# Optimization experiments

Measured on AMD Instinct MI355X. Metric: run time of the kernel, lower is better.

The kernel has to match this reference:

```python
import jax, jax.numpy as jnp
import numpy as np

B, N, D, H = 4, 1024, 1024, 16
NP = N - 1  # prototypes; +1 CLS slot -> n_valid == N
HD = D // H
LN_EPS = 1e-5


def _build_spatial_sim(key):
    centers = jax.random.uniform(key, (NP, 2), dtype=jnp.float32) * 10.0
    diff = centers[:, None, :] - centers[None, :, :]
    d2 = jnp.sum(diff * diff, axis=-1)           # squared pairwise distance
    dist = jnp.sqrt(d2)
    sigma = dist.mean()                           # spatial_sigma = mean cdist
    sim = jnp.exp(-d2 / (2.0 * sigma * sigma))
    sim = sim / sim.max()
    ext = jnp.zeros((NP + 1, NP + 1), dtype=jnp.float32)
    ext = ext.at[0, :].set(1.0).at[:, 0].set(1.0).at[1:, 1:].set(sim)
    return ext


def setup_inputs() -> dict:
    key = jax.random.key(0)
    kc, kx, kq, kp = jax.random.split(key, 4)
    spatial_sim = _build_spatial_sim(kc)          # [N, N] buffer
    x = jax.random.normal(kx, (B, N, D), dtype=jnp.float32)
    gamma = jnp.ones((D,), dtype=jnp.float32)
    beta = jnp.zeros((D,), dtype=jnp.float32)
    w_qkv = jax.random.normal(kq, (D, 3 * D), dtype=jnp.float32) * 0.02
    w_proj = jax.random.normal(kp, (D, D), dtype=jnp.float32) * 0.02
    b_proj = jnp.zeros((D,), dtype=jnp.float32)
    swl = jnp.float32(np.log(0.3 / 0.7))          # inverse_sigmoid(0.3)
    return {"x": x, "gamma": gamma, "beta": beta, "w_qkv": w_qkv,
            "w_proj": w_proj, "b_proj": b_proj,
            "spatial_weight_logit": swl, "spatial_sim": spatial_sim}


def reference(x, gamma, beta, w_qkv, w_proj, b_proj, spatial_weight_logit, spatial_sim):
    b, n, d = x.shape
    scale = HD ** (-0.5)
    # LayerNorm (biased variance, eps=1e-5)
    mu = x.mean(axis=-1, keepdims=True)
    var = jnp.mean((x - mu) ** 2, axis=-1, keepdims=True)
    x_norm = (x - mu) / jnp.sqrt(var + LN_EPS) * gamma + beta
    # QKV projection -> [B, H, N, HD] each
    qkv = (x_norm @ w_qkv).reshape(b, n, 3, H, HD)
    qkv = jnp.transpose(qkv, (2, 0, 3, 1, 4))
    q, k, v = qkv[0], qkv[1], qkv[2]
    scores = jnp.einsum('bhnd,bhmd->bhnm', q, k) * scale
    alpha = jax.nn.sigmoid(spatial_weight_logit)
    # blend feature attention with fixed spatial similarity, then softmax
    attn = jax.nn.softmax((1.0 - alpha) * scores + alpha * spatial_sim[None, None], axis=-1)
    out = jnp.einsum('bhnm,bhmd->bhnd', attn, v)
    out = jnp.transpose(out, (0, 2, 1, 3)).reshape(b, n, d)
    out = out @ w_proj + b_proj
    return x + out
```

## Files before the change

kernel.cpp:

```cpp
#include <hip/hip_runtime.h>

#define Bz 4
#define Nn 1024
#define Dd 1024
#define Hh 16
#define HD 64
#define SCALE 0.125f
#define LN_EPS 1e-5f

typedef __attribute__((ext_vector_type(8))) __bf16 bf16x8;
typedef __attribute__((ext_vector_type(4))) float f32x4;

static __device__ inline unsigned short f2bf(float f) {
    unsigned int u = __float_as_uint(f);
    u += 0x7fffu + ((u >> 16) & 1u);
    return (unsigned short)(u >> 16);
}

static __device__ inline float bf2f(unsigned short s) {
    return __uint_as_float((unsigned)s << 16);
}

static __device__ inline bf16x8 ldfrag(const unsigned short* p) {
    return *(const bf16x8*)p;
}

static __device__ __forceinline__ void glds16(const unsigned short* g, unsigned short* l) {
    __builtin_amdgcn_global_load_lds((const __attribute__((address_space(1))) void*)g,
                                     (__attribute__((address_space(3))) void*)l, 16, 0, 0);
}

__global__ __launch_bounds__(256) void ln_kernel(const float* __restrict__ x,
                                                 const float* __restrict__ gamma,
                                                 const float* __restrict__ beta,
                                                 unsigned short* __restrict__ xn) {
    int row = blockIdx.x;
    int t = threadIdx.x;
    const float* xr = x + (size_t)row * Dd;
    float4 v = ((const float4*)xr)[t];
    float s = v.x + v.y + v.z + v.w;
    float ss = v.x * v.x + v.y * v.y + v.z * v.z + v.w * v.w;
    for (int o = 32; o > 0; o >>= 1) {
        s += __shfl_down(s, o);
        ss += __shfl_down(ss, o);
    }
    __shared__ float red[8];
    int wid = t >> 6;
    if ((t & 63) == 0) { red[wid * 2] = s; red[wid * 2 + 1] = ss; }
    __syncthreads();
    float tot = red[0] + red[2] + red[4] + red[6];
    float tot2 = red[1] + red[3] + red[5] + red[7];
    float mu = tot * (1.0f / Dd);
    float var = tot2 * (1.0f / Dd) - mu * mu;
    float inv = rsqrtf(var + LN_EPS);
    float4 g = ((const float4*)gamma)[t];
    float4 b = ((const float4*)beta)[t];
    ushort4 o4;
    o4.x = f2bf((v.x - mu) * inv * g.x + b.x);
    o4.y = f2bf((v.y - mu) * inv * g.y + b.y);
    o4.z = f2bf((v.z - mu) * inv * g.z + b.z);
    o4.w = f2bf((v.w - mu) * inv * g.w + b.w);
    ((ushort4*)(xn + (size_t)row * Dd))[t] = o4;
}

__global__ __launch_bounds__(256) void transpose_bf16(const float* __restrict__ in,
                                                      unsigned short* __restrict__ out,
                                                      int rows, int cols) {
    __shared__ float tile[32][33];
    int c0 = blockIdx.x * 32, r0 = blockIdx.y * 32;
    int tx = threadIdx.x, ty = threadIdx.y;
    for (int i = 0; i < 32; i += 8)
        tile[ty + i][tx] = in[(size_t)(r0 + ty + i) * cols + c0 + tx];
    __syncthreads();
    for (int i = 0; i < 32; i += 8)
        out[(size_t)(c0 + ty + i) * rows + r0 + tx] = f2bf(tile[tx][ty + i]);
}

__global__ __launch_bounds__(256) void conv_bf16(const float* __restrict__ in,
                                                 unsigned short* __restrict__ out) {
    int i = blockIdx.x * 256 + threadIdx.x;
    float4 v = ((const float4*)in)[i];
    ushort4 o;
    o.x = f2bf(v.x); o.y = f2bf(v.y); o.z = f2bf(v.z); o.w = f2bf(v.w);
    ((ushort4*)out)[i] = o;
}

__global__ __launch_bounds__(256) void gemm_qkv(const unsigned short* __restrict__ A,
                                                const unsigned short* __restrict__ Bt,
                                                unsigned short* __restrict__ qb,
                                                unsigned short* __restrict__ kb,
                                                unsigned short* __restrict__ vtb) {
    __shared__ unsigned short sA[4096], sB[4096];
    int tid = threadIdx.x;
    int w = tid >> 6, lane = tid & 63, lrow = lane & 15, quad = lane >> 4;
    int wm = w >> 1, wn = w & 1;
    int rowbase = blockIdx.y * 128;
    int colbase = blockIdx.x * 128;

    int srow = tid >> 2;
    int kcl = tid & 3;
    int kcg = (kcl - (srow >> 1)) & 3;
    const unsigned short* gA0 = A + (size_t)(rowbase + srow) * 1024 + kcg * 8;
    const unsigned short* gA1 = gA0 + (size_t)64 * 1024;
    const unsigned short* gB0 = Bt + (size_t)(colbase + srow) * 1024 + kcg * 8;
    const unsigned short* gB1 = gB0 + (size_t)64 * 1024;
    unsigned short* lA = sA + w * 512;
    unsigned short* lB = sB + w * 512;

    int ssw = (quad + (lrow >> 1)) & 3;
    const unsigned short* fa = sA + (wm * 64 + lrow) * 32 + ssw * 8;
    const unsigned short* fb = sB + (wn * 64 + lrow) * 32 + ssw * 8;

    f32x4 acc[4][4];
    #pragma unroll
    for (int i = 0; i < 4; i++)
        #pragma unroll
        for (int j = 0; j < 4; j++)
            acc[i][j] = (f32x4){0.f, 0.f, 0.f, 0.f};

    for (int k0 = 0; k0 < 1024; k0 += 32) {
        __syncthreads();
        glds16(gA0 + k0, lA);
        glds16(gA1 + k0, lA + 2048);
        glds16(gB0 + k0, lB);
        glds16(gB1 + k0, lB + 2048);
        __syncthreads();
        bf16x8 a[4], b[4];
        #pragma unroll
        for (int i = 0; i < 4; i++) a[i] = *(const bf16x8*)(fa + i * 512);
        #pragma unroll
        for (int j = 0; j < 4; j++) b[j] = *(const bf16x8*)(fb + j * 512);
        #pragma unroll
        for (int i = 0; i < 4; i++)
            #pragma unroll
            for (int j = 0; j < 4; j++)
                acc[i][j] = __builtin_amdgcn_mfma_f32_16x16x32_bf16(a[i], b[j], acc[i][j], 0, 0, 0);
    }

    #pragma unroll
    for (int j = 0; j < 4; j++) {
        int col = colbase + wn * 64 + j * 16 + lrow;
        int s = col >> 10, rem = col & 1023;
        int h = rem >> 6, e = rem & 63;
        #pragma unroll
        for (int i = 0; i < 4; i++) {
            #pragma unroll
            for (int r = 0; r < 4; r++) {
                int R = rowbase + wm * 64 + i * 16 + quad * 4 + r;
                int bb = R >> 10, n = R & 1023;
                unsigned short val = f2bf(acc[i][j][r]);
                if (s == 0)
                    qb[(((size_t)(bb * Hh + h)) * Nn + n) * HD + e] = val;
                else if (s == 1)
                    kb[(((size_t)(bb * Hh + h)) * Nn + n) * HD + e] = val;
                else
                    vtb[(((size_t)(bb * Hh + h)) * HD + e) * Nn + n] = val;
            }
        }
    }
}

__global__ __launch_bounds__(256) void gemm_proj(const unsigned short* __restrict__ A,
                                                 const unsigned short* __restrict__ Bt,
                                                 const float* __restrict__ bias,
                                                 const float* __restrict__ x,
                                                 float* __restrict__ out) {
    __shared__ unsigned short sA[4096], sB[4096];
    int tid = threadIdx.x;
    int w = tid >> 6, lane = tid & 63, lrow = lane & 15, quad = lane >> 4;
    int wm = w >> 1, wn = w & 1;
    int rowbase = blockIdx.y * 128;
    int colbase = blockIdx.x * 128;

    int srow = tid >> 2;
    int kcl = tid & 3;
    int kcg = (kcl - (srow >> 1)) & 3;
    const unsigned short* gA0 = A + (size_t)(rowbase + srow) * 1024 + kcg * 8;
    const unsigned short* gA1 = gA0 + (size_t)64 * 1024;
    const unsigned short* gB0 = Bt + (size_t)(colbase + srow) * 1024 + kcg * 8;
    const unsigned short* gB1 = gB0 + (size_t)64 * 1024;
    unsigned short* lA = sA + w * 512;
    unsigned short* lB = sB + w * 512;

    int ssw = (quad + (lrow >> 1)) & 3;
    const unsigned short* fa = sA + (wm * 64 + lrow) * 32 + ssw * 8;
    const unsigned short* fb = sB + (wn * 64 + lrow) * 32 + ssw * 8;

    f32x4 acc[4][4];
    #pragma unroll
    for (int i = 0; i < 4; i++)
        #pragma unroll
        for (int j = 0; j < 4; j++)
            acc[i][j] = (f32x4){0.f, 0.f, 0.f, 0.f};

    for (int k0 = 0; k0 < 1024; k0 += 32) {
        __syncthreads();
        glds16(gA0 + k0, lA);
        glds16(gA1 + k0, lA + 2048);
        glds16(gB0 + k0, lB);
        glds16(gB1 + k0, lB + 2048);
        __syncthreads();
        bf16x8 a[4], b[4];
        #pragma unroll
        for (int i = 0; i < 4; i++) a[i] = *(const bf16x8*)(fa + i * 512);
        #pragma unroll
        for (int j = 0; j < 4; j++) b[j] = *(const bf16x8*)(fb + j * 512);
        #pragma unroll
        for (int i = 0; i < 4; i++)
            #pragma unroll
            for (int j = 0; j < 4; j++)
                acc[i][j] = __builtin_amdgcn_mfma_f32_16x16x32_bf16(a[i], b[j], acc[i][j], 0, 0, 0);
    }

    #pragma unroll
    for (int j = 0; j < 4; j++) {
        int col = colbase + wn * 64 + j * 16 + lrow;
        float bc = bias[col];
        #pragma unroll
        for (int i = 0; i < 4; i++) {
            #pragma unroll
            for (int r = 0; r < 4; r++) {
                int R = rowbase + wm * 64 + i * 16 + quad * 4 + r;
                out[(size_t)R * 1024 + col] = acc[i][j][r] + bc + x[(size_t)R * 1024 + col];
            }
        }
    }
}

#define PSTR 72
__global__ __launch_bounds__(256) void attn_kernel(const unsigned short* __restrict__ qb,
                                                   const unsigned short* __restrict__ kb,
                                                   const unsigned short* __restrict__ vtb,
                                                   const unsigned short* __restrict__ simb,
                                                   const float* __restrict__ swl,
                                                   unsigned short* __restrict__ aout) {
    int h = blockIdx.y, bb = blockIdx.z;
    int n0 = blockIdx.x * 128;
    int tid = threadIdx.x;
    int w = tid >> 6, lane = tid & 63;
    int lrow = lane & 15, quad = lane >> 4;
    const unsigned short* q = qb + ((size_t)(bb * Hh + h)) * Nn * HD;
    const unsigned short* k = kb + ((size_t)(bb * Hh + h)) * Nn * HD;
    const unsigned short* vt = vtb + ((size_t)(bb * Hh + h)) * HD * Nn;
    float alpha = 1.f / (1.f + __expf(-swl[0]));
    float c1 = (1.f - alpha) * SCALE;

    __shared__ unsigned short sK[4096];
    __shared__ unsigned short sV[4096];
    __shared__ unsigned short sP[128 * PSTR];

    int qr0 = n0 + w * 32;
    bf16x8 qf[2][2];
    #pragma unroll
    for (int g = 0; g < 2; g++) {
        qf[g][0] = ldfrag(q + (size_t)(qr0 + g * 16 + lrow) * HD + quad * 8);
        qf[g][1] = ldfrag(q + (size_t)(qr0 + g * 16 + lrow) * HD + 32 + quad * 8);
    }

    f32x4 o[2][4];
    #pragma unroll
    for (int g = 0; g < 2; g++)
        #pragma unroll
        for (int et = 0; et < 4; et++) o[g][et] = (f32x4){0.f, 0.f, 0.f, 0.f};
    float rsum[2] = {0.f, 0.f};

    int bs0 = (quad + (lrow >> 1)) & 7;
    int bs1 = (4 + quad + (lrow >> 1)) & 7;
    unsigned short* sPw = sP + (w * 32) * PSTR;

    for (int m0 = 0; m0 < 1024; m0 += 64) {
        __syncthreads();
        #pragma unroll
        for (int i = 0; i < 2; i++) {
            int slot = i * 256 + tid;
            int row = slot >> 3;
            int cg = ((slot & 7) - (row >> 1)) & 7;
            glds16(k + (size_t)(m0 + row) * HD + cg * 8, sK + i * 2048 + w * 512);
        }
        #pragma unroll
        for (int i = 0; i < 2; i++) {
            int slot = i * 256 + tid;
            int row = slot >> 3;
            int cg = ((slot & 7) - (row >> 1)) & 7;
            glds16(vt + (size_t)row * Nn + m0 + cg * 8, sV + i * 2048 + w * 512);
        }
        ushort4 sm[4][2];
        #pragma unroll
        for (int ks = 0; ks < 4; ks++)
            #pragma unroll
            for (int g = 0; g < 2; g++)
                sm[ks][g] = *(const ushort4*)(simb + (size_t)(qr0 + g * 16 + lrow) * Nn
                                              + m0 + ks * 16 + quad * 4);
        __syncthreads();

        #pragma unroll
        for (int ks = 0; ks < 4; ks++) {
            const unsigned short* kr = sK + (ks * 16 + lrow) * 64;
            bf16x8 ak0 = *(const bf16x8*)(kr + bs0 * 8);
            bf16x8 ak1 = *(const bf16x8*)(kr + bs1 * 8);
            #pragma unroll
            for (int g = 0; g < 2; g++) {
                f32x4 c = (f32x4){0.f, 0.f, 0.f, 0.f};
                c = __builtin_amdgcn_mfma_f32_16x16x32_bf16(ak0, qf[g][0], c, 0, 0, 0);
                c = __builtin_amdgcn_mfma_f32_16x16x32_bf16(ak1, qf[g][1], c, 0, 0, 0);
                const unsigned short* smp = (const unsigned short*)&sm[ks][g];
                float e0 = __expf(c1 * c[0] + alpha * bf2f(smp[0]));
                float e1 = __expf(c1 * c[1] + alpha * bf2f(smp[1]));
                float e2 = __expf(c1 * c[2] + alpha * bf2f(smp[2]));
                float e3 = __expf(c1 * c[3] + alpha * bf2f(smp[3]));
                rsum[g] += (e0 + e1) + (e2 + e3);
                uint2 pk;
                pk.x = (__float_as_uint(e0) >> 16) | (__float_as_uint(e1) & 0xffff0000u);
                pk.y = (__float_as_uint(e2) >> 16) | (__float_as_uint(e3) & 0xffff0000u);
                *(uint2*)(sPw + (g * 16 + lrow) * PSTR + ks * 16 + quad * 4) = pk;
            }
        }

        #pragma unroll
        for (int ms = 0; ms < 2; ms++) {
            bf16x8 pa[2];
            #pragma unroll
            for (int g = 0; g < 2; g++)
                pa[g] = *(const bf16x8*)(sPw + (g * 16 + lrow) * PSTR + ms * 32 + quad * 8);
            #pragma unroll
            for (int et = 0; et < 4; et++) {
                int e = et * 16 + lrow;
                int slot = (ms * 4 + quad + (e >> 1)) & 7;
                bf16x8 vb = *(const bf16x8*)(sV + e * 64 + slot * 8);
                #pragma unroll
                for (int g = 0; g < 2; g++)
                    o[g][et] = __builtin_amdgcn_mfma_f32_16x16x32_bf16(pa[g], vb, o[g][et], 0, 0, 0);
            }
        }
    }

    #pragma unroll
    for (int g = 0; g < 2; g++) {
        rsum[g] += __shfl_xor(rsum[g], 16);
        rsum[g] += __shfl_xor(rsum[g], 32);
    }

    #pragma unroll
    for (int g = 0; g < 2; g++)
        #pragma unroll
        for (int r = 0; r < 4; r++) {
            float inv = 1.f / __shfl(rsum[g], quad * 4 + r);
            int qn = qr0 + g * 16 + quad * 4 + r;
            #pragma unroll
            for (int et = 0; et < 4; et++)
                aout[((size_t)bb * Nn + qn) * Dd + h * HD + et * 16 + lrow]
                    = f2bf(o[g][et][r] * inv);
        }
}

extern "C" void kernel_launch(void* const* d_in, const int* in_sizes, int n_in,
                              void* d_out, int out_size, void* d_ws, size_t ws_size,
                              hipStream_t stream) {
    const float* x      = (const float*)d_in[0];
    const float* gamma  = (const float*)d_in[1];
    const float* beta   = (const float*)d_in[2];
    const float* w_qkv  = (const float*)d_in[3];
    const float* w_proj = (const float*)d_in[4];
    const float* b_proj = (const float*)d_in[5];
    const float* swl    = (const float*)d_in[6];
    const float* sim    = (const float*)d_in[7];
    float* out = (float*)d_out;

    unsigned short* ws = (unsigned short*)d_ws;
    unsigned short* xn     = ws;
    unsigned short* wqkvT  = xn + 4194304;
    unsigned short* wprojT = wqkvT + 3145728;
    unsigned short* qb     = wprojT + 1048576;
    unsigned short* kb     = qb + 4194304;
    unsigned short* vtb    = kb + 4194304;
    unsigned short* aout   = vtb + 4194304;
    unsigned short* simb   = xn;

    transpose_bf16<<<dim3(3072 / 32, 1024 / 32), dim3(32, 8), 0, stream>>>(w_qkv, wqkvT, 1024, 3072);
    transpose_bf16<<<dim3(1024 / 32, 1024 / 32), dim3(32, 8), 0, stream>>>(w_proj, wprojT, 1024, 1024);
    ln_kernel<<<4096, 256, 0, stream>>>(x, gamma, beta, xn);
    gemm_qkv<<<dim3(24, 32), 256, 0, stream>>>(xn, wqkvT, qb, kb, vtb);
    conv_bf16<<<1024, 256, 0, stream>>>(sim, simb);
    attn_kernel<<<dim3(8, 16, 4), 256, 0, stream>>>(qb, kb, vtb, simb, swl, aout);
    gemm_proj<<<dim3(8, 32), 256, 0, stream>>>(aout, wprojT, b_proj, x, out);
}
```

Before: 231.5 us.

## Double GEMM K-tile to 64 and stage V-transpose stores through LDS

Both GEMM kernels now load a 64-wide K slice per iteration (twice the shared memory) with an 8-chunk swizzle. This halves the number of barrier pairs and global-to-LDS round trips per output tile. The QKV kernel also splits its epilogue: Q/K blocks write directly, while V blocks transpose through LDS so the transposed V stores become contiguous 8-byte writes instead of scattered 2-byte ones. The larger LDS footprint may lower occupancy.

```diff
diff --git a/kernel.cpp b/kernel.cpp
--- a/kernel.cpp
+++ b/kernel.cpp
@@ -85,31 +85,30 @@
     ((ushort4*)out)[i] = o;
 }
 
+
 __global__ __launch_bounds__(256) void gemm_qkv(const unsigned short* __restrict__ A,
                                                 const unsigned short* __restrict__ Bt,
                                                 unsigned short* __restrict__ qb,
                                                 unsigned short* __restrict__ kb,
                                                 unsigned short* __restrict__ vtb) {
-    __shared__ unsigned short sA[4096], sB[4096];
+    __shared__ unsigned short sA[8192], sB[8192];
     int tid = threadIdx.x;
     int w = tid >> 6, lane = tid & 63, lrow = lane & 15, quad = lane >> 4;
     int wm = w >> 1, wn = w & 1;
     int rowbase = blockIdx.y * 128;
     int colbase = blockIdx.x * 128;
 
-    int srow = tid >> 2;
-    int kcl = tid & 3;
-    int kcg = (kcl - (srow >> 1)) & 3;
-    const unsigned short* gA0 = A + (size_t)(rowbase + srow) * 1024 + kcg * 8;
-    const unsigned short* gA1 = gA0 + (size_t)64 * 1024;
-    const unsigned short* gB0 = Bt + (size_t)(colbase + srow) * 1024 + kcg * 8;
-    const unsigned short* gB1 = gB0 + (size_t)64 * 1024;
+    int srow = tid >> 3;
+    int gch = ((tid & 7) - (srow >> 1)) & 7;
+    const unsigned short* gA = A + (size_t)(rowbase + srow) * 1024 + gch * 8;
+    const unsigned short* gB = Bt + (size_t)(colbase + srow) * 1024 + gch * 8;
     unsigned short* lA = sA + w * 512;
     unsigned short* lB = sB + w * 512;
 
-    int ssw = (quad + (lrow >> 1)) & 3;
-    const unsigned short* fa = sA + (wm * 64 + lrow) * 32 + ssw * 8;
-    const unsigned short* fb = sB + (wn * 64 + lrow) * 32 + ssw * 8;
+    int bs0 = ((quad + (lrow >> 1)) & 7) * 8;
+    int bs1 = ((4 + quad + (lrow >> 1)) & 7) * 8;
+    const unsigned short* fa = sA + (wm * 64 + lrow) * 64;
+    const unsigned short* fb = sB + (wn * 64 + lrow) * 64;
 
     f32x4 acc[4][4];
     #pragma unroll
@@ -118,43 +117,70 @@
         for (int j = 0; j < 4; j++)
             acc[i][j] = (f32x4){0.f, 0.f, 0.f, 0.f};
 
-    for (int k0 = 0; k0 < 1024; k0 += 32) {
-        __syncthreads();
-        glds16(gA0 + k0, lA);
-        glds16(gA1 + k0, lA + 2048);
-        glds16(gB0 + k0, lB);
-        glds16(gB1 + k0, lB + 2048);
-        __syncthreads();
-        bf16x8 a[4], b[4];
-        #pragma unroll
-        for (int i = 0; i < 4; i++) a[i] = *(const bf16x8*)(fa + i * 512);
-        #pragma unroll
-        for (int j = 0; j < 4; j++) b[j] = *(const bf16x8*)(fb + j * 512);
-        #pragma unroll
-        for (int i = 0; i < 4; i++)
-            #pragma unroll
-            for (int j = 0; j < 4; j++)
-                acc[i][j] = __builtin_amdgcn_mfma_f32_16x16x32_bf16(a[i], b[j], acc[i][j], 0, 0, 0);
-    }
-
-    #pragma unroll
-    for (int j = 0; j < 4; j++) {
-        int col = colbase + wn * 64 + j * 16 + lrow;
-        int s = col >> 10, rem = col & 1023;
-        int h = rem >> 6, e = rem & 63;
-        #pragma unroll
-        for (int i = 0; i < 4; i++) {
-            #pragma unroll
-            for (int r = 0; r < 4; r++) {
-                int R = rowbase + wm * 64 + i * 16 + quad * 4 + r;
-                int bb = R >> 10, n = R & 1023;
-                unsigned short val = f2bf(acc[i][j][r]);
-                if (s == 0)
-                    qb[(((size_t)(bb * Hh + h)) * Nn + n) * HD + e] = val;
-                else if (s == 1)
-                    kb[(((size_t)(bb * Hh + h)) * Nn + n) * HD + e] = val;
-                else
-                    vtb[(((size_t)(bb * Hh + h)) * HD + e) * Nn + n] = val;
+    for (int k0 = 0; k0 < 1024; k0 += 64) {
+        __syncthreads();
+        #pragma unroll
+        for (int c = 0; c < 4; c++) {
+            glds16(gA + (size_t)c * 32768 + k0, lA + c * 2048);
+            glds16(gB + (size_t)c * 32768 + k0, lB + c * 2048);
+        }
+        __syncthreads();
+        #pragma unroll
+        for (int s = 0; s < 2; s++) {
+            int bo = s ? bs1 : bs0;
+            bf16x8 a[4], b[4];
+            #pragma unroll
+            for (int i = 0; i < 4; i++) a[i] = *(const bf16x8*)(fa + i * 1024 + bo);
+            #pragma unroll
+            for (int j = 0; j < 4; j++) b[j] = *(const bf16x8*)(fb + j * 1024 + bo);
+            #pragma unroll
+            for (int i = 0; i < 4; i++)
+                #pragma unroll
+                for (int j = 0; j < 4; j++)
+                    acc[i][j] = __builtin_amdgcn_mfma_f32_16x16x32_bf16(a[i], b[j], acc[i][j], 0, 0, 0);
+        }
+    }
+
+    if (colbase < 2048) {
+        #pragma unroll
+        for (int j = 0; j < 4; j++) {
+            int col = colbase + wn * 64 + j * 16 + lrow;
+            int s = col >> 10, rem = col & 1023;
+            int h = rem >> 6, e = rem & 63;
+            unsigned short* dst = (s == 0) ? qb : kb;
+            #pragma unroll
+            for (int i = 0; i < 4; i++) {
+                #pragma unroll
+                for (int r = 0; r < 4; r++) {
+                    int R = rowbase + wm * 64 + i * 16 + quad * 4 + r;
+                    int bb = R >> 10, n = R & 1023;
+                    dst[(((size_t)(bb * Hh + h)) * Nn + n) * HD + e] = f2bf(acc[i][j][r]);
+                }
+            }
+        }
+    } else {
+        int bb = rowbase >> 10;
+        int nbase = (rowbase & 1023) + wm * 64;
+        unsigned short* sc = sA + w * 2048;
+        int er = lane >> 2, nc = lane & 3;
+        #pragma unroll
+        for (int j = 0; j < 4; j++) {
+            __syncthreads();
+            int ebase = colbase + wn * 64 + j * 16 - 2048;
+            int h = ebase >> 6, e0 = ebase & 63;
+            #pragma unroll
+            for (int i = 0; i < 4; i++) {
+                uint2 pk;
+                pk.x = (unsigned)f2bf(acc[i][j][0]) | ((unsigned)f2bf(acc[i][j][1]) << 16);
+                pk.y = (unsigned)f2bf(acc[i][j][2]) | ((unsigned)f2bf(acc[i][j][3]) << 16);
+                *(uint2*)(sc + lrow * 68 + i * 16 + quad * 4) = pk;
+            }
+            __syncthreads();
+            unsigned short* vrow = vtb + ((size_t)((bb * Hh + h) * HD) + e0 + er) * Nn + nbase;
+            #pragma unroll
+            for (int c = 0; c < 4; c++) {
+                uint2 v = *(const uint2*)(sc + er * 68 + c * 16 + nc * 4);
+                *(uint2*)(vrow + c * 16 + nc * 4) = v;
             }
         }
     }
@@ -165,26 +191,24 @@
                                                  const float* __restrict__ bias,
                                                  const float* __restrict__ x,
                                                  float* __restrict__ out) {
-    __shared__ unsigned short sA[4096], sB[4096];
+    __shared__ unsigned short sA[8192], sB[8192];
     int tid = threadIdx.x;
     int w = tid >> 6, lane = tid & 63, lrow = lane & 15, quad = lane >> 4;
     int wm = w >> 1, wn = w & 1;
     int rowbase = blockIdx.y * 128;
     int colbase = blockIdx.x * 128;
 
-    int srow = tid >> 2;
-    int kcl = tid & 3;
-    int kcg = (kcl - (srow >> 1)) & 3;
-    const unsigned short* gA0 = A + (size_t)(rowbase + srow) * 1024 + kcg * 8;
-    const unsigned short* gA1 = gA0 + (size_t)64 * 1024;
-    const unsigned short* gB0 = Bt + (size_t)(colbase + srow) * 1024 + kcg * 8;
-    const unsigned short* gB1 = gB0 + (size_t)64 * 1024;
+    int srow = tid >> 3;
+    int gch = ((tid & 7) - (srow >> 1)) & 7;
+    const unsigned short* gA = A + (size_t)(rowbase + srow) * 1024 + gch * 8;
+    const unsigned short* gB = Bt + (size_t)(colbase + srow) * 1024 + gch * 8;
     unsigned short* lA = sA + w * 512;
     unsigned short* lB = sB + w * 512;
 
-    int ssw = (quad + (lrow >> 1)) & 3;
-    const unsigned short* fa = sA + (wm * 64 + lrow) * 32 + ssw * 8;
-    const unsigned short* fb = sB + (wn * 64 + lrow) * 32 + ssw * 8;
+    int bs0 = ((quad + (lrow >> 1)) & 7) * 8;
+    int bs1 = ((4 + quad + (lrow >> 1)) & 7) * 8;
+    const unsigned short* fa = sA + (wm * 64 + lrow) * 64;
+    const unsigned short* fb = sB + (wn * 64 + lrow) * 64;
 
     f32x4 acc[4][4];
     #pragma unroll
@@ -193,23 +217,28 @@
         for (int j = 0; j < 4; j++)
             acc[i][j] = (f32x4){0.f, 0.f, 0.f, 0.f};
 
-    for (int k0 = 0; k0 < 1024; k0 += 32) {
-        __syncthreads();
-        glds16(gA0 + k0, lA);
-        glds16(gA1 + k0, lA + 2048);
-        glds16(gB0 + k0, lB);
-        glds16(gB1 + k0, lB + 2048);
-        __syncthreads();
-        bf16x8 a[4], b[4];
-        #pragma unroll
-        for (int i = 0; i < 4; i++) a[i] = *(const bf16x8*)(fa + i * 512);
-        #pragma unroll
-        for (int j = 0; j < 4; j++) b[j] = *(const bf16x8*)(fb + j * 512);
-        #pragma unroll
-        for (int i = 0; i < 4; i++)
-            #pragma unroll
-            for (int j = 0; j < 4; j++)
-                acc[i][j] = __builtin_amdgcn_mfma_f32_16x16x32_bf16(a[i], b[j], acc[i][j], 0, 0, 0);
+    for (int k0 = 0; k0 < 1024; k0 += 64) {
+        __syncthreads();
+        #pragma unroll
+        for (int c = 0; c < 4; c++) {
+            glds16(gA + (size_t)c * 32768 + k0, lA + c * 2048);
+            glds16(gB + (size_t)c * 32768 + k0, lB + c * 2048);
+        }
+        __syncthreads();
+        #pragma unroll
+        for (int s = 0; s < 2; s++) {
+            int bo = s ? bs1 : bs0;
+            bf16x8 a[4], b[4];
+            #pragma unroll
+            for (int i = 0; i < 4; i++) a[i] = *(const bf16x8*)(fa + i * 1024 + bo);
+            #pragma unroll
+            for (int j = 0; j < 4; j++) b[j] = *(const bf16x8*)(fb + j * 1024 + bo);
+            #pragma unroll
+            for (int i = 0; i < 4; i++)
+                #pragma unroll
+                for (int j = 0; j < 4; j++)
+                    acc[i][j] = __builtin_amdgcn_mfma_f32_16x16x32_bf16(a[i], b[j], acc[i][j], 0, 0, 0);
+        }
     }
 
     #pragma unroll
```

New measurement: 206.0 us. 1.12x faster.

## Double-buffer LDS tiles in GEMMs and attention, stage V-transpose stores through LDS

Applied to the files above, without the earlier changes.

Converts the K-loops of gemm_qkv, gemm_proj and attn_kernel to a two-stage LDS ping-pong. The next tile's global-to-LDS copy, and in attention the next block's spatial-sim registers, are issued before computing on the current tile, with one barrier per iteration instead of two. This is meant to hide global load latency behind MFMA work. The V part of the QKV epilogue now transposes each tile through LDS so the transposed V writes go out as contiguous 8-byte rows instead of scattered 2-byte stores. In exchange it doubles LDS per block, which may reduce occupancy, and it relies on the async LDS loads having completed before the single barrier.

```diff
diff --git a/kernel.cpp b/kernel.cpp
--- a/kernel.cpp
+++ b/kernel.cpp
@@ -85,12 +85,13 @@
     ((ushort4*)out)[i] = o;
 }
 
+
 __global__ __launch_bounds__(256) void gemm_qkv(const unsigned short* __restrict__ A,
                                                 const unsigned short* __restrict__ Bt,
                                                 unsigned short* __restrict__ qb,
                                                 unsigned short* __restrict__ kb,
                                                 unsigned short* __restrict__ vtb) {
-    __shared__ unsigned short sA[4096], sB[4096];
+    __shared__ unsigned short sA[8192], sB[8192];
     int tid = threadIdx.x;
     int w = tid >> 6, lane = tid & 63, lrow = lane & 15, quad = lane >> 4;
     int wm = w >> 1, wn = w & 1;
@@ -108,8 +109,8 @@
     unsigned short* lB = sB + w * 512;
 
     int ssw = (quad + (lrow >> 1)) & 3;
-    const unsigned short* fa = sA + (wm * 64 + lrow) * 32 + ssw * 8;
-    const unsigned short* fb = sB + (wn * 64 + lrow) * 32 + ssw * 8;
+    const unsigned short* fa0 = sA + (wm * 64 + lrow) * 32 + ssw * 8;
+    const unsigned short* fb0 = sB + (wn * 64 + lrow) * 32 + ssw * 8;
 
     f32x4 acc[4][4];
     #pragma unroll
@@ -118,13 +119,24 @@
         for (int j = 0; j < 4; j++)
             acc[i][j] = (f32x4){0.f, 0.f, 0.f, 0.f};
 
-    for (int k0 = 0; k0 < 1024; k0 += 32) {
+    glds16(gA0, lA);
+    glds16(gA1, lA + 2048);
+    glds16(gB0, lB);
+    glds16(gB1, lB + 2048);
+
+    for (int it = 0; it < 32; it++) {
+        int cb = it & 1;
         __syncthreads();
-        glds16(gA0 + k0, lA);
-        glds16(gA1 + k0, lA + 2048);
-        glds16(gB0 + k0, lB);
-        glds16(gB1 + k0, lB + 2048);
-        __syncthreads();
+        if (it < 31) {
+            int k0 = (it + 1) * 32;
+            int bo = (cb ^ 1) * 4096;
+            glds16(gA0 + k0, lA + bo);
+            glds16(gA1 + k0, lA + bo + 2048);
+            glds16(gB0 + k0, lB + bo);
+            glds16(gB1 + k0, lB + bo + 2048);
+        }
+        const unsigned short* fa = fa0 + cb * 4096;
+        const unsigned short* fb = fb0 + cb * 4096;
         bf16x8 a[4], b[4];
         #pragma unroll
         for (int i = 0; i < 4; i++) a[i] = *(const bf16x8*)(fa + i * 512);
@@ -137,24 +149,46 @@
                 acc[i][j] = __builtin_amdgcn_mfma_f32_16x16x32_bf16(a[i], b[j], acc[i][j], 0, 0, 0);
     }
 
-    #pragma unroll
-    for (int j = 0; j < 4; j++) {
-        int col = colbase + wn * 64 + j * 16 + lrow;
-        int s = col >> 10, rem = col & 1023;
-        int h = rem >> 6, e = rem & 63;
-        #pragma unroll
-        for (int i = 0; i < 4; i++) {
-            #pragma unroll
-            for (int r = 0; r < 4; r++) {
-                int R = rowbase + wm * 64 + i * 16 + quad * 4 + r;
-                int bb = R >> 10, n = R & 1023;
-                unsigned short val = f2bf(acc[i][j][r]);
-                if (s == 0)
-                    qb[(((size_t)(bb * Hh + h)) * Nn + n) * HD + e] = val;
-                else if (s == 1)
-                    kb[(((size_t)(bb * Hh + h)) * Nn + n) * HD + e] = val;
-                else
-                    vtb[(((size_t)(bb * Hh + h)) * HD + e) * Nn + n] = val;
+    if (colbase < 2048) {
+        #pragma unroll
+        for (int j = 0; j < 4; j++) {
+            int col = colbase + wn * 64 + j * 16 + lrow;
+            int s = col >> 10, rem = col & 1023;
+            int h = rem >> 6, e = rem & 63;
+            unsigned short* dst = (s == 0) ? qb : kb;
+            #pragma unroll
+            for (int i = 0; i < 4; i++) {
+                #pragma unroll
+                for (int r = 0; r < 4; r++) {
+                    int R = rowbase + wm * 64 + i * 16 + quad * 4 + r;
+                    int bb = R >> 10, n = R & 1023;
+                    dst[(((size_t)(bb * Hh + h)) * Nn + n) * HD + e] = f2bf(acc[i][j][r]);
+                }
+            }
+        }
+    } else {
+        int bb = rowbase >> 10;
+        int nbase = (rowbase & 1023) + wm * 64;
+        unsigned short* sc = sA + w * 2048;
+        int er = lane >> 2, nc = lane & 3;
+        #pragma unroll
+        for (int j = 0; j < 4; j++) {
+            __syncthreads();
+            int ebase = colbase + wn * 64 + j * 16 - 2048;
+            int h = ebase >> 6, e0 = ebase & 63;
+            #pragma unroll
+            for (int i = 0; i < 4; i++) {
+                uint2 pk;
+                pk.x = (unsigned)f2bf(acc[i][j][0]) | ((unsigned)f2bf(acc[i][j][1]) << 16);
+                pk.y = (unsigned)f2bf(acc[i][j][2]) | ((unsigned)f2bf(acc[i][j][3]) << 16);
+                *(uint2*)(sc + lrow * 68 + i * 16 + quad * 4) = pk;
+            }
+            __syncthreads();
+            unsigned short* vrow = vtb + ((size_t)((bb * Hh + h) * HD) + e0 + er) * Nn + nbase;
+            #pragma unroll
+            for (int c = 0; c < 4; c++) {
+                uint2 v = *(const uint2*)(sc + er * 68 + c * 16 + nc * 4);
+                *(uint2*)(vrow + c * 16 + nc * 4) = v;
             }
         }
     }
@@ -165,7 +199,7 @@
                                                  const float* __restrict__ bias,
                                                  const float* __restrict__ x,
                                                  float* __restrict__ out) {
-    __shared__ unsigned short sA[4096], sB[4096];
+    __shared__ unsigned short sA[8192], sB[8192];
     int tid = threadIdx.x;
     int w = tid >> 6, lane = tid & 63, lrow = lane & 15, quad = lane >> 4;
     int wm = w >> 1, wn = w & 1;
@@ -183,8 +217,8 @@
     unsigned short* lB = sB + w * 512;
 
     int ssw = (quad + (lrow >> 1)) & 3;
-    const unsigned short* fa = sA + (wm * 64 + lrow) * 32 + ssw * 8;
-    const unsigned short* fb = sB + (wn * 64 + lrow) * 32 + ssw * 8;
+    const unsigned short* fa0 = sA + (wm * 64 + lrow) * 32 + ssw * 8;
+    const unsigned short* fb0 = sB + (wn * 64 + lrow) * 32 + ssw * 8;
 
     f32x4 acc[4][4];
     #pragma unroll
@@ -193,13 +227,24 @@
         for (int j = 0; j < 4; j++)
             acc[i][j] = (f32x4){0.f, 0.f, 0.f, 0.f};
 
-    for (int k0 = 0; k0 < 1024; k0 += 32) {
+    glds16(gA0, lA);
+    glds16(gA1, lA + 2048);
+    glds16(gB0, lB);
+    glds16(gB1, lB + 2048);
+
+    for (int it = 0; it < 32; it++) {
+        int cb = it & 1;
         __syncthreads();
-        glds16(gA0 + k0, lA);
-        glds16(gA1 + k0, lA + 2048);
-        glds16(gB0 + k0, lB);
-        glds16(gB1 + k0, lB + 2048);
-        __syncthreads();
+        if (it < 31) {
+            int k0 = (it + 1) * 32;
+            int bo = (cb ^ 1) * 4096;
+            glds16(gA0 + k0, lA + bo);
+            glds16(gA1 + k0, lA + bo + 2048);
+            glds16(gB0 + k0, lB + bo);
+            glds16(gB1 + k0, lB + bo + 2048);
+        }
+        const unsigned short* fa = fa0 + cb * 4096;
+        const unsigned short* fb = fb0 + cb * 4096;
         bf16x8 a[4], b[4];
         #pragma unroll
         for (int i = 0; i < 4; i++) a[i] = *(const bf16x8*)(fa + i * 512);
@@ -245,8 +290,8 @@
     float alpha = 1.f / (1.f + __expf(-swl[0]));
     float c1 = (1.f - alpha) * SCALE;
 
-    __shared__ unsigned short sK[4096];
-    __shared__ unsigned short sV[4096];
+    __shared__ unsigned short sK[8192];
+    __shared__ unsigned short sV[8192];
     __shared__ unsigned short sP[128 * PSTR];
 
     int qr0 = n0 + w * 32;
@@ -268,34 +313,46 @@
     int bs1 = (4 + quad + (lrow >> 1)) & 7;
     unsigned short* sPw = sP + (w * 32) * PSTR;
 
-    for (int m0 = 0; m0 < 1024; m0 += 64) {
+    int srow0 = tid >> 3, cg0 = ((tid & 7) - (srow0 >> 1)) & 7;
+    int srow1 = (256 + tid) >> 3, cg1 = ((tid & 7) - (srow1 >> 1)) & 7;
+    const unsigned short* simrow0 = simb + (size_t)(qr0 + lrow) * Nn + quad * 4;
+    const unsigned short* simrow1 = simb + (size_t)(qr0 + 16 + lrow) * Nn + quad * 4;
+
+    ushort4 smc[4][2], smn[4][2];
+
+    glds16(k + (size_t)srow0 * HD + cg0 * 8, sK + w * 512);
+    glds16(k + (size_t)srow1 * HD + cg1 * 8, sK + 2048 + w * 512);
+    glds16(vt + (size_t)srow0 * Nn + cg0 * 8, sV + w * 512);
+    glds16(vt + (size_t)srow1 * Nn + cg1 * 8, sV + 2048 + w * 512);
+    #pragma unroll
+    for (int ks = 0; ks < 4; ks++) {
+        smc[ks][0] = *(const ushort4*)(simrow0 + ks * 16);
+        smc[ks][1] = *(const ushort4*)(simrow1 + ks * 16);
+    }
+
+    for (int mt = 0; mt < 16; mt++) {
+        int cb = mt & 1;
         __syncthreads();
-        #pragma unroll
-        for (int i = 0; i < 2; i++) {
-            int slot = i * 256 + tid;
-            int row = slot >> 3;
-            int cg = ((slot & 7) - (row >> 1)) & 7;
-            glds16(k + (size_t)(m0 + row) * HD + cg * 8, sK + i * 2048 + w * 512);
-        }
-        #pragma unroll
-        for (int i = 0; i < 2; i++) {
-            int slot = i * 256 + tid;
-            int row = slot >> 3;
-            int cg = ((slot & 7) - (row >> 1)) & 7;
-            glds16(vt + (size_t)row * Nn + m0 + cg * 8, sV + i * 2048 + w * 512);
-        }
-        ushort4 sm[4][2];
-        #pragma unroll
-        for (int ks = 0; ks < 4; ks++)
-            #pragma unroll
-            for (int g = 0; g < 2; g++)
-                sm[ks][g] = *(const ushort4*)(simb + (size_t)(qr0 + g * 16 + lrow) * Nn
-                                              + m0 + ks * 16 + quad * 4);
-        __syncthreads();
+        if (mt < 15) {
+            int m0 = (mt + 1) * 64;
+            int bo = (cb ^ 1) * 4096;
+            glds16(k + (size_t)(m0 + srow0) * HD + cg0 * 8, sK + bo + w * 512);
+            glds16(k + (size_t)(m0 + srow1) * HD + cg1 * 8, sK + bo + 2048 + w * 512);
+            glds16(vt + (size_t)srow0 * Nn + m0 + cg0 * 8, sV + bo + w * 512);
+            glds16(vt + (size_t)srow1 * Nn + m0 + cg1 * 8, sV + bo + 2048 + w * 512);
+            #pragma unroll
+            for (int ks = 0; ks < 4; ks++) {
+                smn[ks][0] = *(const ushort4*)(simrow0 + m0 + ks * 16);
+                smn[ks][1] = *(const ushort4*)(simrow1 + m0 + ks * 16);
+            }
+        }
+
+        const unsigned short* sKc = sK + cb * 4096;
+        const unsigned short* sVc = sV + cb * 4096;
 
         #pragma unroll
         for (int ks = 0; ks < 4; ks++) {
-            const unsigned short* kr = sK + (ks * 16 + lrow) * 64;
+            const unsigned short* kr = sKc + (ks * 16 + lrow) * 64;
             bf16x8 ak0 = *(const bf16x8*)(kr + bs0 * 8);
             bf16x8 ak1 = *(const bf16x8*)(kr + bs1 * 8);
             #pragma unroll
@@ -303,7 +360,7 @@
                 f32x4 c = (f32x4){0.f, 0.f, 0.f, 0.f};
                 c = __builtin_amdgcn_mfma_f32_16x16x32_bf16(ak0, qf[g][0], c, 0, 0, 0);
                 c = __builtin_amdgcn_mfma_f32_16x16x32_bf16(ak1, qf[g][1], c, 0, 0, 0);
-                const unsigned short* smp = (const unsigned short*)&sm[ks][g];
+                const unsigned short* smp = (const unsigned short*)&smc[ks][g];
                 float e0 = __expf(c1 * c[0] + alpha * bf2f(smp[0]));
                 float e1 = __expf(c1 * c[1] + alpha * bf2f(smp[1]));
                 float e2 = __expf(c1 * c[2] + alpha * bf2f(smp[2]));
@@ -326,11 +383,17 @@
             for (int et = 0; et < 4; et++) {
                 int e = et * 16 + lrow;
                 int slot = (ms * 4 + quad + (e >> 1)) & 7;
-                bf16x8 vb = *(const bf16x8*)(sV + e * 64 + slot * 8);
+                bf16x8 vb = *(const bf16x8*)(sVc + e * 64 + slot * 8);
                 #pragma unroll
                 for (int g = 0; g < 2; g++)
                     o[g][et] = __builtin_amdgcn_mfma_f32_16x16x32_bf16(pa[g], vb, o[g][et], 0, 0, 0);
             }
+        }
+
+        #pragma unroll
+        for (int ks = 0; ks < 4; ks++) {
+            smc[ks][0] = smn[ks][0];
+            smc[ks][1] = smn[ks][1];
         }
     }
 
```

New measurement: 226.9 us. 2.0% less time.
